# Kernel tuning notes

Hardware: AMD Instinct MI355X
Metric: run time of the kernel (lower is better)

## Reference

```python
import jax, jax.numpy as jnp
import numpy as np

R = 16      # num_rels
NB = 16     # num_bases
N2 = 8192   # dp2 neighbours (layer-0 sampled nodes)
N1 = 1024   # dp1 neighbours (layer-1 sampled nodes)
NOUT = 256  # output batch nodes
F = 128     # feat_size
E = 64      # embed_size
C = 32      # num_classes


def setup_inputs() -> dict:
    key = jax.random.key(0)
    ks = jax.random.split(key, 8)
    g = lambda k, sh, scale: jax.random.normal(k, sh, dtype=jnp.float32) * scale
    return {
        "X_batch": g(ks[0], (N2, F), 1.0),
        "sel_idx": jnp.arange(N2, dtype=jnp.int64) if jax.config.jax_enable_x64 else jnp.arange(N2, dtype=jnp.int32),
        "A0": g(ks[1], (N1, R * N2), 1.0 / np.sqrt(R * N2)),
        "A1": g(ks[2], (NOUT, R * N1), 1.0 / np.sqrt(R * N1)),
        "comp1": g(ks[3], (R, NB), 1.0 / np.sqrt(NB)),
        "bases1": g(ks[4], (NB, F, E), 1.0 / np.sqrt(F)),
        "comp2": g(ks[5], (R, NB), 1.0 / np.sqrt(NB)),
        "bases2": g(ks[6], (NB, E, C), 1.0 / np.sqrt(E)),
        "bias1": jnp.zeros((E,), jnp.float32),
        "bias2": jnp.zeros((C,), jnp.float32),
    }


def reference(X_batch, sel_idx, A0, A1, comp1, bases1, comp2, bases2, bias1, bias2):
    # gather the rows of X_batch corresponding to dp2 neighbours
    x = X_batch[sel_idx]                                  # [N2, F]
    # layer 1: basis-composed relation weights, relation-stacked matmul
    w1 = jnp.einsum('rb,beh->reh', comp1, bases1)         # [R, F, E]
    xw = jnp.einsum('ne,reh->rnh', x, w1)                 # [R, N2, E]
    h1 = A0 @ xw.reshape(R * N2, E)                       # [N1, E]
    h1 = jax.nn.relu(h1 + bias1)
    # layer 2
    w2 = jnp.einsum('rb,bho->rho', comp2, bases2)         # [R, E, C]
    h2 = jnp.einsum('nh,rhc->rnc', h1, w2)                # [R, N1, C]
    out = A1 @ h2.reshape(R * N1, C) + bias2              # [NOUT, C]
    return out
```

## Files before the change

kernel.cpp:

```cpp
#include <hip/hip_runtime.h>

#define RR_ 16
#define N2_ 8192
#define N1_ 1024
#define NOUT_ 256
#define F_ 128
#define E_ 64
#define C_ 32
#define KBIG_ 131072

typedef __attribute__((ext_vector_type(4))) float f32x4;
typedef __attribute__((ext_vector_type(8))) short short8;
typedef __attribute__((ext_vector_type(4))) short s16x4;

#define MFMA(a,b,c) __builtin_amdgcn_mfma_f32_16x16x32_bf16((a),(b),(c),0,0,0)

__device__ __forceinline__ unsigned short f2bf(float f) {
  unsigned int u = __builtin_bit_cast(unsigned int, f);
  u += 0x7fffu + ((u >> 16) & 1u);
  return (unsigned short)(u >> 16);
}

__device__ __forceinline__ short8 cvt8(f32x4 v0, f32x4 v1) {
  short8 r;
  r[0] = (short)f2bf(v0[0]); r[1] = (short)f2bf(v0[1]);
  r[2] = (short)f2bf(v0[2]); r[3] = (short)f2bf(v0[3]);
  r[4] = (short)f2bf(v1[0]); r[5] = (short)f2bf(v1[1]);
  r[6] = (short)f2bf(v1[2]); r[7] = (short)f2bf(v1[3]);
  return r;
}

__global__ __launch_bounds__(256) void k_prep(
    const float* __restrict__ comp1, const float* __restrict__ bases1,
    const float* __restrict__ comp2, const float* __restrict__ bases2,
    short* __restrict__ w1T, short* __restrict__ w2T)
{
  int bid = blockIdx.x, t = threadIdx.x;
  if (bid < 32) {
    int base = bid * 4096;
    for (int i = 0; i < 16; ++i) {
      int e = base + i * 256 + t;
      int r = e >> 13, rem = e & 8191;
      int h = rem >> 7, f = rem & 127;
      float s = 0.f;
      #pragma unroll
      for (int b = 0; b < 16; ++b) s += comp1[r * 16 + b] * bases1[b * 8192 + f * 64 + h];
      w1T[e] = (short)f2bf(s);
    }
  } else {
    int base = (bid - 32) * 4096;
    for (int i = 0; i < 16; ++i) {
      int e = base + i * 256 + t;
      int r = e >> 11, rem = e & 2047;
      int c = rem >> 6, h = rem & 63;
      float s = 0.f;
      #pragma unroll
      for (int b = 0; b < 16; ++b) s += comp2[r * 16 + b] * bases2[b * 2048 + h * 32 + c];
      w2T[e] = (short)f2bf(s);
    }
  }
}

__global__ __launch_bounds__(256) void k_xw(
    const float* __restrict__ X, const int* __restrict__ sel,
    const short* __restrict__ w1T, short* __restrict__ xwT)
{
  int w = blockIdx.x * 4 + (threadIdx.x >> 6);
  int lane = threadIdx.x & 63, lr = lane & 15, lg = lane >> 4;
  int r = w >> 8;
  int n0 = (w & 255) * 32;

  bool is64 = (sel[1] == 0 && sel[2] == 1);
  int i0 = is64 ? sel[2 * (n0 + lr)] : sel[n0 + lr];
  int i1 = is64 ? sel[2 * (n0 + 16 + lr)] : sel[n0 + 16 + lr];

  const short* aBase = w1T + r * 8192 + lr * 128 + 8 * lg;
  const float* b0p = X + (size_t)i0 * 128 + 8 * lg;
  const float* b1p = X + (size_t)i1 * 128 + 8 * lg;

  f32x4 acc[4][2] = {};
  #pragma unroll
  for (int ks = 0; ks < 4; ++ks) {
    short8 a[4];
    #pragma unroll
    for (int mf = 0; mf < 4; ++mf)
      a[mf] = *(const short8*)(aBase + mf * 2048 + ks * 32);
    short8 b[2];
    b[0] = cvt8(*(const f32x4*)(b0p + ks * 32), *(const f32x4*)(b0p + ks * 32 + 4));
    b[1] = cvt8(*(const f32x4*)(b1p + ks * 32), *(const f32x4*)(b1p + ks * 32 + 4));
    #pragma unroll
    for (int mf = 0; mf < 4; ++mf)
      #pragma unroll
      for (int nf = 0; nf < 2; ++nf)
        acc[mf][nf] = MFMA(a[mf], b[nf], acc[mf][nf]);
  }
  #pragma unroll
  for (int mf = 0; mf < 4; ++mf)
    #pragma unroll
    for (int nf = 0; nf < 2; ++nf)
      #pragma unroll
      for (int rr = 0; rr < 4; ++rr) {
        int h = mf * 16 + 4 * lg + rr;
        int col = r * 8192 + n0 + nf * 16 + lr;
        xwT[(size_t)h * KBIG_ + col] = (short)f2bf(acc[mf][nf][rr]);
      }
}

__device__ __forceinline__ void stageA(const float* aRow0, int s, int lane,
                                       float* ldsBase) {
  const float* rbase = aRow0 + (size_t)s * 256;
  #pragma unroll
  for (int j = 0; j < 16; ++j) {
    const float* gp = rbase + (size_t)j * KBIG_ +
        ((((unsigned)lane * 16u) ^ (((unsigned)j & 7u) << 4)) >> 2);
    __builtin_amdgcn_global_load_lds(
        (const __attribute__((address_space(1))) void*)gp,
        (__attribute__((address_space(3))) void*)(ldsBase + j * 256), 16, 0, 0);
  }
}

__global__ __launch_bounds__(256) void k_h1(
    const float* __restrict__ A0, const short* __restrict__ xwT,
    float* __restrict__ h1p)
{
  __shared__ float As[4][2][16][256];
  const int tid  = threadIdx.x;
  const int w    = tid >> 6;
  const int lane = tid & 63, lr = lane & 15, lg = lane >> 4;
  const int mt = blockIdx.x >> 4;
  const int ch = blockIdx.x & 15;
  const int m0 = mt * 64 + w * 16;
  const size_t kc = (size_t)ch * 8192;

  const float* aRow0 = A0 + (size_t)m0 * KBIG_ + kc;
  const short* bb    = xwT + (size_t)lr * KBIG_ + kc + 8 * lg;
  float* myLds0 = &As[w][0][0][0];
  float* myLds1 = &As[w][1][0][0];

  f32x4 acc[4] = {};
  const unsigned swz = (unsigned)(lr & 7) * 4;

  stageA(aRow0, 0, lane, myLds0);

  for (int s = 0; s < 32; ++s) {
    float* cur = (s & 1) ? myLds1 : myLds0;
    float* nxt = (s & 1) ? myLds0 : myLds1;

    short8 b[8][4];
    #pragma unroll
    for (int ks = 0; ks < 8; ++ks)
      #pragma unroll
      for (int nf = 0; nf < 4; ++nf)
        b[ks][nf] = *(const short8*)(bb + (size_t)nf * 16 * KBIG_ + s * 256 + ks * 32);
    __builtin_amdgcn_sched_barrier(0);

    if (s + 1 < 32) {
      stageA(aRow0, s + 1, lane, nxt);
      asm volatile("s_waitcnt vmcnt(16)" ::: "memory");
    } else {
      asm volatile("s_waitcnt vmcnt(0)" ::: "memory");
    }
    __builtin_amdgcn_sched_barrier(0);

    const float* lrow = cur + lr * 256;
    #pragma unroll
    for (int ks = 0; ks < 8; ++ks) {
      unsigned c0 = ((unsigned)(ks * 32 + 8 * lg)) ^ swz;
      unsigned c1 = ((unsigned)(ks * 32 + 8 * lg + 4)) ^ swz;
      f32x4 v0 = *(const f32x4*)(lrow + c0);
      f32x4 v1 = *(const f32x4*)(lrow + c1);
      short8 a = cvt8(v0, v1);
      #pragma unroll
      for (int nf = 0; nf < 4; ++nf)
        acc[nf] = MFMA(a, b[ks][nf], acc[nf]);
    }
  }

  float* basep = h1p + (size_t)ch * 65536 + (size_t)m0 * 64;
  #pragma unroll
  for (int nf = 0; nf < 4; ++nf)
    #pragma unroll
    for (int rr = 0; rr < 4; ++rr)
      basep[(4 * lg + rr) * 64 + nf * 16 + lr] = acc[nf][rr];
}

__global__ __launch_bounds__(256) void k_red(
    const float* __restrict__ h1p, const float* __restrict__ bias1,
    short* __restrict__ h1b)
{
  int e = (blockIdx.x * 256 + threadIdx.x) * 4;
  f32x4 s = {0.f, 0.f, 0.f, 0.f};
  #pragma unroll
  for (int c = 0; c < 16; ++c) {
    f32x4 v = *(const f32x4*)(h1p + (size_t)c * 65536 + e);
    s += v;
  }
  int h = e & 63;
  s16x4 o;
  #pragma unroll
  for (int j = 0; j < 4; ++j) {
    float x = s[j] + bias1[h + j];
    x = x > 0.f ? x : 0.f;
    o[j] = (short)f2bf(x);
  }
  *(s16x4*)(h1b + e) = o;
}

__global__ __launch_bounds__(256) void k_h2(
    const short* __restrict__ w2T, const short* __restrict__ h1b,
    short* __restrict__ H2T)
{
  int w = blockIdx.x * 4 + (threadIdx.x >> 6);
  int lane = threadIdx.x & 63, lr = lane & 15, lg = lane >> 4;
  int r = w >> 4;
  int n0 = (w & 15) * 64;

  f32x4 acc[2][4] = {};
  #pragma unroll
  for (int ks = 0; ks < 2; ++ks) {
    short8 a[2];
    #pragma unroll
    for (int mf = 0; mf < 2; ++mf)
      a[mf] = *(const short8*)(w2T + r * 2048 + (mf * 16 + lr) * 64 + ks * 32 + 8 * lg);
    short8 b[4];
    #pragma unroll
    for (int nf = 0; nf < 4; ++nf)
      b[nf] = *(const short8*)(h1b + (size_t)(n0 + nf * 16 + lr) * 64 + ks * 32 + 8 * lg);
    #pragma unroll
    for (int mf = 0; mf < 2; ++mf)
      #pragma unroll
      for (int nf = 0; nf < 4; ++nf)
        acc[mf][nf] = MFMA(a[mf], b[nf], acc[mf][nf]);
  }
  #pragma unroll
  for (int mf = 0; mf < 2; ++mf)
    #pragma unroll
    for (int nf = 0; nf < 4; ++nf)
      #pragma unroll
      for (int rr = 0; rr < 4; ++rr) {
        int c = mf * 16 + 4 * lg + rr;
        int col = r * 1024 + n0 + nf * 16 + lr;
        H2T[(size_t)c * 16384 + col] = (short)f2bf(acc[mf][nf][rr]);
      }
}

__global__ __launch_bounds__(256) void k_out(
    const float* __restrict__ A1, const short* __restrict__ H2T,
    float* __restrict__ outp)
{
  int w = blockIdx.x * 4 + (threadIdx.x >> 6);
  int lane = threadIdx.x & 63, lr = lane & 15, lg = lane >> 4;
  int mt = w >> 7;
  int ch = w & 127;
  int m0 = mt * 64;
  size_t kc = (size_t)ch * 128;

  const float* aBase = A1 + (size_t)(m0 + lr) * 16384 + kc + 8 * lg;
  const short* bBase = H2T + (size_t)lr * 16384 + kc + 8 * lg;

  f32x4 acc[4][2] = {};
  #pragma unroll
  for (int ks = 0; ks < 4; ++ks) {
    short8 a[4];
    #pragma unroll
    for (int mf = 0; mf < 4; ++mf) {
      const float* p = aBase + (size_t)mf * 16 * 16384 + ks * 32;
      f32x4 v0 = *(const f32x4*)p;
      f32x4 v1 = *((const f32x4*)p + 1);
      a[mf] = cvt8(v0, v1);
    }
    short8 b[2];
    #pragma unroll
    for (int nf = 0; nf < 2; ++nf)
      b[nf] = *(const short8*)(bBase + (size_t)nf * 16 * 16384 + ks * 32);
    #pragma unroll
    for (int mf = 0; mf < 4; ++mf)
      #pragma unroll
      for (int nf = 0; nf < 2; ++nf)
        acc[mf][nf] = MFMA(a[mf], b[nf], acc[mf][nf]);
  }
  float* base = outp + (size_t)ch * 8192;
  #pragma unroll
  for (int mf = 0; mf < 4; ++mf)
    #pragma unroll
    for (int nf = 0; nf < 2; ++nf)
      #pragma unroll
      for (int rr = 0; rr < 4; ++rr)
        base[(m0 + mf * 16 + 4 * lg + rr) * 32 + nf * 16 + lr] = acc[mf][nf][rr];
}

__global__ __launch_bounds__(256) void k_outred(
    const float* __restrict__ outp, const float* __restrict__ bias2,
    float* __restrict__ out)
{
  int e = (blockIdx.x * 256 + threadIdx.x) * 4;
  f32x4 s = {0.f, 0.f, 0.f, 0.f};
  #pragma unroll 8
  for (int c = 0; c < 128; ++c) {
    f32x4 v = *(const f32x4*)(outp + (size_t)c * 8192 + e);
    s += v;
  }
  int cc = e & 31;
  f32x4 o;
  #pragma unroll
  for (int j = 0; j < 4; ++j)
    o[j] = s[j] + bias2[cc + j];
  *(f32x4*)(out + e) = o;
}

extern "C" void kernel_launch(void* const* d_in, const int* in_sizes, int n_in,
                              void* d_out, int out_size, void* d_ws, size_t ws_size,
                              hipStream_t stream) {
  (void)in_sizes; (void)n_in; (void)out_size; (void)ws_size;
  const float* X      = (const float*)d_in[0];
  const int*   sel    = (const int*)  d_in[1];
  const float* A0     = (const float*)d_in[2];
  const float* A1     = (const float*)d_in[3];
  const float* comp1  = (const float*)d_in[4];
  const float* bases1 = (const float*)d_in[5];
  const float* comp2  = (const float*)d_in[6];
  const float* bases2 = (const float*)d_in[7];
  const float* bias1  = (const float*)d_in[8];
  const float* bias2  = (const float*)d_in[9];
  float* out = (float*)d_out;

  char* ws = (char*)d_ws;
  short* w1T = (short*)(ws);
  short* w2T = (short*)(ws + 262144);
  short* xwT = (short*)(ws + 327680);
  float* h1p = (float*)(ws + 17104896);
  short* h1b = (short*)(ws + 50659328);
  short* H2T = (short*)(ws + 50790400);
  float* outp= (float*)(ws + 51838976);

  k_prep  <<<40,   256, 0, stream>>>(comp1, bases1, comp2, bases2, w1T, w2T);
  k_xw    <<<1024, 256, 0, stream>>>(X, sel, w1T, xwT);
  k_h1    <<<256,  256, 0, stream>>>(A0, xwT, h1p);
  k_red   <<<64,   256, 0, stream>>>(h1p, bias1, h1b);
  k_h2    <<<64,   256, 0, stream>>>(w2T, h1b, H2T);
  k_out   <<<128,  256, 0, stream>>>(A1, H2T, outp);
  k_outred<<<8,    256, 0, stream>>>(outp, bias2, out);
}
```

Baseline: 276.1 us.

## Pre-convert A0 to tiled bf16 layout and split K into 64 chunks

Adds a conversion kernel that reads the fp32 A0 adjacency with nontemporal loads and writes a bf16 copy in a tile-contiguous layout. A new h1 kernel then loads A fragments directly from that copy, without LDS staging, and splits K across 64 chunks for more parallelism. The reduction kernel now takes the chunk count as an argument. This path only runs when the workspace is large enough, and it costs an extra full pass over A0: a 512MB read plus a 256MB write, on top of the later read.

After: 387.4 us. 1.4x slower.

```diff
diff --git a/kernel.cpp b/kernel.cpp
--- a/kernel.cpp
+++ b/kernel.cpp
@@ -106,6 +106,59 @@
       }
 }
 
+__global__ __launch_bounds__(256) void k_conv(
+    const float* __restrict__ A0, short* __restrict__ A0bf)
+{
+  int gw = (blockIdx.x * 256 + threadIdx.x) >> 6;
+  int lane = threadIdx.x & 63;
+  for (int i = 0; i < 8; ++i) {
+    int p = i * 8192 + gw;
+    int m = p >> 6, ch = p & 63;
+    int mt = m >> 4, r = m & 15;
+    const float* inb = A0 + (size_t)p * 2048;
+    short* outb = A0bf + ((size_t)(mt * 64 + ch) * 16 + r) * 2048;
+    #pragma unroll
+    for (int j = 0; j < 8; ++j) {
+      f32x4 v = __builtin_nontemporal_load((const f32x4*)(inb + j * 256 + lane * 4));
+      s16x4 o;
+      o[0] = (short)f2bf(v[0]); o[1] = (short)f2bf(v[1]);
+      o[2] = (short)f2bf(v[2]); o[3] = (short)f2bf(v[3]);
+      *(s16x4*)(outb + j * 256 + lane * 4) = o;
+    }
+  }
+}
+
+__global__ __launch_bounds__(256, 4) void k_h1_tiled(
+    const short* __restrict__ A0bf, const short* __restrict__ xwT,
+    float* __restrict__ h1p)
+{
+  int wave = blockIdx.x * 4 + (threadIdx.x >> 6);
+  int lane = threadIdx.x & 63, lr = lane & 15, lg = lane >> 4;
+  int mt = wave >> 6;
+  int ch = wave & 63;
+
+  const short* ab = A0bf + (size_t)(mt * 64 + ch) * 32768 + lr * 2048 + 8 * lg;
+  const short* bb = xwT + (size_t)lr * KBIG_ + ch * 2048 + 8 * lg;
+
+  f32x4 acc[4] = {};
+  #pragma unroll 4
+  for (int kk = 0; kk < 64; ++kk) {
+    short8 a = *(const short8*)(ab + kk * 32);
+    #pragma unroll
+    for (int nf = 0; nf < 4; ++nf) {
+      short8 b = *(const short8*)(bb + (size_t)nf * 16 * KBIG_ + kk * 32);
+      acc[nf] = MFMA(a, b, acc[nf]);
+    }
+  }
+
+  float* basep = h1p + (size_t)ch * 65536;
+  #pragma unroll
+  for (int nf = 0; nf < 4; ++nf)
+    #pragma unroll
+    for (int rr = 0; rr < 4; ++rr)
+      basep[(mt * 16 + 4 * lg + rr) * 64 + nf * 16 + lr] = acc[nf][rr];
+}
+
 __device__ __forceinline__ void stageA(const float* aRow0, int s, int lane,
                                        float* ldsBase) {
   const float* rbase = aRow0 + (size_t)s * 256;
@@ -119,7 +172,7 @@
   }
 }
 
-__global__ __launch_bounds__(256) void k_h1(
+__global__ __launch_bounds__(256) void k_h1_direct(
     const float* __restrict__ A0, const short* __restrict__ xwT,
     float* __restrict__ h1p)
 {
@@ -186,12 +239,12 @@
 
 __global__ __launch_bounds__(256) void k_red(
     const float* __restrict__ h1p, const float* __restrict__ bias1,
-    short* __restrict__ h1b)
+    short* __restrict__ h1b, int nch)
 {
   int e = (blockIdx.x * 256 + threadIdx.x) * 4;
   f32x4 s = {0.f, 0.f, 0.f, 0.f};
-  #pragma unroll
-  for (int c = 0; c < 16; ++c) {
+  #pragma unroll 8
+  for (int c = 0; c < nch; ++c) {
     f32x4 v = *(const f32x4*)(h1p + (size_t)c * 65536 + e);
     s += v;
   }
@@ -311,7 +364,7 @@
 extern "C" void kernel_launch(void* const* d_in, const int* in_sizes, int n_in,
                               void* d_out, int out_size, void* d_ws, size_t ws_size,
                               hipStream_t stream) {
-  (void)in_sizes; (void)n_in; (void)out_size; (void)ws_size;
+  (void)in_sizes; (void)n_in; (void)out_size;
   const float* X      = (const float*)d_in[0];
   const int*   sel    = (const int*)  d_in[1];
   const float* A0     = (const float*)d_in[2];
@@ -329,14 +382,23 @@
   short* w2T = (short*)(ws + 262144);
   short* xwT = (short*)(ws + 327680);
   float* h1p = (float*)(ws + 17104896);
-  short* h1b = (short*)(ws + 50659328);
-  short* H2T = (short*)(ws + 50790400);
-  float* outp= (float*)(ws + 51838976);
+  short* h1b = (short*)(ws + 33882112);
+  short* H2T = (short*)(ws + 34013184);
+  float* outp= (float*)(ws + 35061760);
+  short* A0bf= (short*)(ws + 39256064);
+
+  bool big = ws_size >= (size_t)307691520;
 
   k_prep  <<<40,   256, 0, stream>>>(comp1, bases1, comp2, bases2, w1T, w2T);
   k_xw    <<<1024, 256, 0, stream>>>(X, sel, w1T, xwT);
-  k_h1    <<<256,  256, 0, stream>>>(A0, xwT, h1p);
-  k_red   <<<64,   256, 0, stream>>>(h1p, bias1, h1b);
+  if (big) {
+    k_conv    <<<2048, 256, 0, stream>>>(A0, A0bf);
+    k_h1_tiled<<<1024, 256, 0, stream>>>(A0bf, xwT, h1p);
+    k_red     <<<64,   256, 0, stream>>>(h1p, bias1, h1b, 64);
+  } else {
+    k_h1_direct<<<256, 256, 0, stream>>>(A0, xwT, h1p);
+    k_red      <<<64,  256, 0, stream>>>(h1p, bias1, h1b, 16);
+  }
   k_h2    <<<64,   256, 0, stream>>>(w2T, h1b, H2T);
   k_out   <<<128,  256, 0, stream>>>(A1, H2T, outp);
   k_outred<<<8,    256, 0, stream>>>(outp, bias2, out);
```
